# Performance work log

Hardware: AMD Instinct MI355X
Metric: run time of the kernel (lower is better)

## Reference

```python
import jax, jax.numpy as jnp
import numpy as np

D = 16_777_216        # size of hashed wide-weight array (self.D)
B = 1024              # batch size (sequential samples)
F = 64                # num_total_wide_features (indices per sample)
LR = 0.05             # lr_w set via compile()
L2_DECAY = 1e-6       # L2_decay set via compile()


def setup_inputs() -> dict:
    key = jax.random.key(0)
    k1, k2, k3 = jax.random.split(key, 3)
    X_w_indices = jax.random.randint(k1, (B, F), 0, D, dtype=jnp.int32)
    X_d = jax.random.randint(k2, (B, 3), 0, 1000)                     # unused by forward (deep tower absent)
    y = (jax.random.uniform(k3, (B,)) < 0.5).astype(jnp.float32)      # binary labels
    # model state, as initialized in __init__: w = [0.0]*D, b = 0.0, decay_times = [0]*D, q = 0
    w = jnp.zeros((D,), jnp.float32)
    b = jnp.zeros((), jnp.float32)
    decay_times = jnp.zeros((D,), jnp.int32)
    return {"X_w_indices": X_w_indices, "X_d": X_d, "y": y,
            "w": w, "b": b, "decay_times": decay_times}


def reference(X_w_indices, X_d, y, w, b, decay_times):
    """Sequential wide-side forward with lazy L2 decay + per-sample SGD update.

    Per sample j (state carried across samples, matching the Python loop):
      - lazy-decay touched weights: w[i] *= (1-L2)^(q - decay_times[i])
      - wTx = sum of (decayed) w over index occurrences; z = clip(wTx + b, -35, 35)
      - p = sigmoid(z); g = p - y
      - update: w[i] -= lr*g per occurrence (duplicates accumulate), b -= lr*g, q += 1
    Returns y_pred of shape [B].
    """
    one_minus = jnp.float32(1.0 - L2_DECAY)

    def step(carry, inp):
        w, dt, b, q = carry
        idx, yj = inp                                   # idx: [F] int32
        dec = one_minus ** (q - dt[idx]).astype(jnp.float32)   # lazy decay factors
        wv = w[idx] * dec                                # decayed weight values (dup-safe: same value per dup)
        z = jnp.clip(jnp.sum(wv) + b, -35.0, 35.0)
        p = jax.nn.sigmoid(z)
        g = p - yj
        # write back decayed values once, then scatter-add the SGD step per occurrence
        w = w.at[idx].set(wv).at[idx].add(-LR * g)
        dt = dt.at[idx].set(q)
        return (w, dt, b - LR * g, q + 1), p

    init = (w, decay_times, b, jnp.int32(0))
    (_, _, _, _), y_pred = jax.lax.scan(step, init, (X_w_indices, y))
    return y_pred
```

## Files before the change

### kernel.cpp

```cpp
#include <hip/hip_runtime.h>

#define B     1024
#define F     64
#define NOCC  (B * F)
#define LRW   0.05f
#define LOG2_LAMBDA (-1.4426957e-6f)
#define LN_LAMBDA   (-1.0000005e-6f)

#define TBITS 17
#define TSIZE (1 << TBITS)
#define TMASK (TSIZE - 1)
#define MAXP  16

#define DPP_ADDF(x, ctrl, rmask) \
  __int_as_float(__builtin_amdgcn_update_dpp(0, __float_as_int(x), (ctrl), (rmask), 0xF, false))

__global__ void __launch_bounds__(256)
wd_base_insert(const int* __restrict__ Xw,
               const float* __restrict__ w0,
               const int* __restrict__ dt0,
               float* __restrict__ S0,
               int* __restrict__ tkey,
               int* __restrict__ thead,
               int* __restrict__ tnext,
               int* __restrict__ tslot) {
    if (blockIdx.x < B / 4) {
        int j = blockIdx.x * 4 + (threadIdx.x >> 6);
        int lane = threadIdx.x & 63;
        int idx = Xw[j * F + lane];
        float wv = w0[idx];
        int dt = dt0[idx];
        float dec = exp2f((float)(j - dt) * LOG2_LAMBDA);
        float v = wv * dec;
        #pragma unroll
        for (int off = 32; off; off >>= 1) v += __shfl_xor(v, off, 64);
        if (lane == 0) S0[j] = v;
    } else {
        int o = (blockIdx.x - B / 4) * 256 + threadIdx.x;
        if (o >= NOCC) return;
        int idx = Xw[o];
        unsigned h = ((unsigned)idx * 2654435761u) >> (32 - TBITS);
        for (;;) {
            int prev = atomicCAS(&tkey[h], -1, idx);
            if (prev == -1 || prev == idx) break;
            h = (h + 1) & TMASK;
        }
        tslot[o] = (int)h;
        tnext[o] = atomicExch(&thead[h], o);
    }
}

__global__ void wd_pairs(const int* __restrict__ tslot,
                         const int* __restrict__ thead,
                         const int* __restrict__ tnext,
                         int* __restrict__ cnt,
                         int* __restrict__ pairs) {
    int o = blockIdx.x * blockDim.x + threadIdx.x;
    if (o >= NOCC) return;
    int j = o >> 6;
    int cur = thead[tslot[o]];
    while (cur != -1) {
        int k = cur >> 6;
        if (k < j) {
            int t = atomicAdd(&cnt[j], 1);
            if (t < MAXP) pairs[j * MAXP + t] = k;
        }
        cur = tnext[cur];
    }
}

__global__ void __launch_bounds__(256)
wd_seq(const float* __restrict__ S0,
       const int* __restrict__ cnt,
       const int* __restrict__ pairs,
       const float* __restrict__ y,
       const float* __restrict__ b0,
       float* __restrict__ out) {
    __shared__ float sS[B], sy[B], sg[B];
    __shared__ int   sc[B];
    __shared__ int   sp[B * 4];

    int t = threadIdx.x;
    for (int j = t; j < B; j += 256) {
        sS[j] = S0[j];
        sy[j] = y[j];
        sg[j] = 0.0f;
        int c = cnt[j];
        if (c > MAXP) c = MAXP;
        sc[j] = c;
        #pragma unroll
        for (int q = 0; q < 4; ++q) sp[j * 4 + q] = pairs[j * MAXP + q];
    }
    __syncthreads();
    if (t >= 64) return;

    int lane = t;
    float bc = b0[0];

    for (int ch = 0; ch < 16; ++ch) {
        int j = ch * 64 + lane;
        float S0j = sS[j], yj = sy[j];
        int c = sc[j];
        int k0 = (c > 0) ? sp[j * 4 + 0] : j;
        int k1 = (c > 1) ? sp[j * 4 + 1] : j;
        int k2 = (c > 2) ? sp[j * 4 + 2] : j;
        int k3 = (c > 3) ? sp[j * 4 + 3] : j;
        float d0 = (c > 0) ? fmaf((float)(j - k0), LN_LAMBDA, 1.0f) : 0.0f;
        float d1 = (c > 1) ? fmaf((float)(j - k1), LN_LAMBDA, 1.0f) : 0.0f;
        float d2 = (c > 2) ? fmaf((float)(j - k2), LN_LAMBDA, 1.0f) : 0.0f;
        float d3 = (c > 3) ? fmaf((float)(j - k3), LN_LAMBDA, 1.0f) : 0.0f;

        float corrv = 0.0f;
        if (c > 0) {
            corrv = d0 * sg[k0] + d1 * sg[k1] + d2 * sg[k2] + d3 * sg[k3];
        }

        float delta = 0.0f, p = 0.5f, g = 0.0f, incl = 0.0f;
        for (int it = 0; it < 14; ++it) {
            float z = fmaf(-LRW, corrv, S0j) + bc + delta;
            z = fminf(35.0f, fmaxf(-35.0f, z));
            p = __fdividef(1.0f, 1.0f + __expf(-z));
            g = p - yj;
            sg[j] = g;
            float nc = 0.0f;
            if (c > 0) {
                nc = d0 * sg[k0] + d1 * sg[k1]
                   + d2 * sg[k2] + d3 * sg[k3];
                for (int q = 4; q < c; ++q) {
                    int k = pairs[j * MAXP + q];
                    nc = fmaf(fmaf((float)(j - k), LN_LAMBDA, 1.0f), sg[k], nc);
                }
            }
            incl = g;
            incl += DPP_ADDF(incl, 0x111, 0xF);
            incl += DPP_ADDF(incl, 0x112, 0xF);
            incl += DPP_ADDF(incl, 0x114, 0xF);
            incl += DPP_ADDF(incl, 0x118, 0xF);
            incl += DPP_ADDF(incl, 0x142, 0xA);
            incl += DPP_ADDF(incl, 0x143, 0xC);
            delta = -LRW * (incl - g);
            corrv = nc;
        }
        out[j] = p;
        bc = fmaf(-LRW, __shfl(incl, 63, 64), bc);
    }
}

extern "C" void kernel_launch(void* const* d_in, const int* in_sizes, int n_in,
                              void* d_out, int out_size, void* d_ws, size_t ws_size,
                              hipStream_t stream) {
    const int*   Xw  = (const int*)d_in[0];
    const float* y   = (const float*)d_in[2];
    const float* w0  = (const float*)d_in[3];
    const float* b0  = (const float*)d_in[4];
    const int*   dt0 = (const int*)d_in[5];
    float* out = (float*)d_out;

    float* S0    = (float*)d_ws;
    int*   cnt   = (int*)(S0 + B);
    int*   pairs = cnt + B;
    int*   tkey  = pairs + B * MAXP;
    int*   thead = tkey + TSIZE;
    int*   tnext = thead + TSIZE;
    int*   tslot = tnext + NOCC;

    hipMemsetAsync(tkey, 0xFF, (size_t)2 * TSIZE * sizeof(int), stream);
    hipMemsetAsync(cnt, 0, (size_t)B * sizeof(int), stream);

    wd_base_insert<<<B / 4 + NOCC / 256, 256, 0, stream>>>(
        Xw, w0, dt0, S0, tkey, thead, tnext, tslot);
    wd_pairs<<<NOCC / 256, 256, 0, stream>>>(tslot, thead, tnext, cnt, pairs);
    wd_seq<<<1, 256, 0, stream>>>(S0, cnt, pairs, y, b0, out);
}
```

Measured before the change: 194.4 us.

## Split in-chunk and prior-chunk corrections, use shuffles, cut fixed-point iterations

The sequential wave now precomputes, once per 64-sample chunk, the gradient corrections coming from earlier chunks. Corrections from samples inside the current chunk are read with wavefront shuffles instead of shared-memory round trips, and the slow path for more than four pairs only runs when some lane needs it. The fixed-point iteration count drops from 14 to 8, and the counter memset is folded into the first kernel. Fewer iterations could leave long in-chunk dependency chains unconverged, which risks accuracy when collisions chain.

```diff
diff --git a/kernel.cpp b/kernel.cpp
--- a/kernel.cpp
+++ b/kernel.cpp
@@ -11,6 +11,7 @@
 #define TSIZE (1 << TBITS)
 #define TMASK (TSIZE - 1)
 #define MAXP  16
+#define NIT   8
 
 #define DPP_ADDF(x, ctrl, rmask) \
   __int_as_float(__builtin_amdgcn_update_dpp(0, __float_as_int(x), (ctrl), (rmask), 0xF, false))
@@ -23,8 +24,13 @@
                int* __restrict__ tkey,
                int* __restrict__ thead,
                int* __restrict__ tnext,
-               int* __restrict__ tslot) {
+               int* __restrict__ tslot,
+               int* __restrict__ cnt) {
     if (blockIdx.x < B / 4) {
+        if (blockIdx.x == 0) {
+            #pragma unroll
+            for (int q = 0; q < 4; ++q) cnt[threadIdx.x * 4 + q] = 0;
+        }
         int j = blockIdx.x * 4 + (threadIdx.x >> 6);
         int lane = threadIdx.x & 63;
         int idx = Xw[j * F + lane];
@@ -84,7 +90,6 @@
     for (int j = t; j < B; j += 256) {
         sS[j] = S0[j];
         sy[j] = y[j];
-        sg[j] = 0.0f;
         int c = cnt[j];
         if (c > MAXP) c = MAXP;
         sc[j] = c;
@@ -99,38 +104,49 @@
 
     for (int ch = 0; ch < 16; ++ch) {
         int j = ch * 64 + lane;
+        int base = ch * 64;
         float S0j = sS[j], yj = sy[j];
         int c = sc[j];
-        int k0 = (c > 0) ? sp[j * 4 + 0] : j;
-        int k1 = (c > 1) ? sp[j * 4 + 1] : j;
-        int k2 = (c > 2) ? sp[j * 4 + 2] : j;
-        int k3 = (c > 3) ? sp[j * 4 + 3] : j;
-        float d0 = (c > 0) ? fmaf((float)(j - k0), LN_LAMBDA, 1.0f) : 0.0f;
-        float d1 = (c > 1) ? fmaf((float)(j - k1), LN_LAMBDA, 1.0f) : 0.0f;
-        float d2 = (c > 2) ? fmaf((float)(j - k2), LN_LAMBDA, 1.0f) : 0.0f;
-        float d3 = (c > 3) ? fmaf((float)(j - k3), LN_LAMBDA, 1.0f) : 0.0f;
 
-        float corrv = 0.0f;
-        if (c > 0) {
-            corrv = d0 * sg[k0] + d1 * sg[k1] + d2 * sg[k2] + d3 * sg[k3];
+        float corr_pre = 0.0f;
+        float dIn[4];
+        int   lIn[4];
+        bool  anyin = false;
+        #pragma unroll
+        for (int q = 0; q < 4; ++q) {
+            int k = sp[j * 4 + q];
+            bool valid = (q < c);
+            float d = fmaf((float)(j - k), LN_LAMBDA, 1.0f);
+            bool inch = valid && (k >= base);
+            dIn[q] = inch ? d : 0.0f;
+            lIn[q] = inch ? (k - base) : lane;
+            if (valid && !inch) corr_pre = fmaf(d, sg[k], corr_pre);
+            anyin |= inch;
         }
+        bool waveIn  = __any(anyin);
+        bool waveBig = __any(c > 4);
 
-        float delta = 0.0f, p = 0.5f, g = 0.0f, incl = 0.0f;
-        for (int it = 0; it < 14; ++it) {
-            float z = fmaf(-LRW, corrv, S0j) + bc + delta;
+        float g = 0.0f, delta = 0.0f, p = 0.5f, incl = 0.0f;
+        float zb = S0j + bc;
+        for (int it = 0; it < NIT; ++it) {
+            float corrv = corr_pre;
+            if (waveIn) {
+                corrv = fmaf(dIn[0], __shfl(g, lIn[0], 64), corrv);
+                corrv = fmaf(dIn[1], __shfl(g, lIn[1], 64), corrv);
+                corrv = fmaf(dIn[2], __shfl(g, lIn[2], 64), corrv);
+                corrv = fmaf(dIn[3], __shfl(g, lIn[3], 64), corrv);
+            }
+            if (waveBig) {
+                sg[j] = g;
+                for (int q = 4; q < c; ++q) {
+                    int k = pairs[j * MAXP + q];
+                    corrv = fmaf(fmaf((float)(j - k), LN_LAMBDA, 1.0f), sg[k], corrv);
+                }
+            }
+            float z = fmaf(-LRW, corrv, zb) + delta;
             z = fminf(35.0f, fmaxf(-35.0f, z));
             p = __fdividef(1.0f, 1.0f + __expf(-z));
             g = p - yj;
-            sg[j] = g;
-            float nc = 0.0f;
-            if (c > 0) {
-                nc = d0 * sg[k0] + d1 * sg[k1]
-                   + d2 * sg[k2] + d3 * sg[k3];
-                for (int q = 4; q < c; ++q) {
-                    int k = pairs[j * MAXP + q];
-                    nc = fmaf(fmaf((float)(j - k), LN_LAMBDA, 1.0f), sg[k], nc);
-                }
-            }
             incl = g;
             incl += DPP_ADDF(incl, 0x111, 0xF);
             incl += DPP_ADDF(incl, 0x112, 0xF);
@@ -139,9 +155,9 @@
             incl += DPP_ADDF(incl, 0x142, 0xA);
             incl += DPP_ADDF(incl, 0x143, 0xC);
             delta = -LRW * (incl - g);
-            corrv = nc;
         }
         out[j] = p;
+        sg[j] = g;
         bc = fmaf(-LRW, __shfl(incl, 63, 64), bc);
     }
 }
@@ -165,10 +181,9 @@
     int*   tslot = tnext + NOCC;
 
     hipMemsetAsync(tkey, 0xFF, (size_t)2 * TSIZE * sizeof(int), stream);
-    hipMemsetAsync(cnt, 0, (size_t)B * sizeof(int), stream);
 
     wd_base_insert<<<B / 4 + NOCC / 256, 256, 0, stream>>>(
-        Xw, w0, dt0, S0, tkey, thead, tnext, tslot);
+        Xw, w0, dt0, S0, tkey, thead, tnext, tslot, cnt);
     wd_pairs<<<NOCC / 256, 256, 0, stream>>>(tslot, thead, tnext, cnt, pairs);
     wd_seq<<<1, 256, 0, stream>>>(S0, cnt, pairs, y, b0, out);
 }
```

After: 178.6 us. 8.1% less time.
